# Kernel optimization log

Hardware: AMD Instinct MI355X
Metric: run time of the kernel (lower is better)

## Reference

```python
import jax, jax.numpy as jnp
import numpy as np

N, E = 20000, 320000
IN, HID, R, HEADS = 128, 256, 4, 4
C = HID // HEADS  # per-head dim


def setup_inputs() -> dict:
    key = jax.random.key(0)
    ks = jax.random.split(key, 20)
    g = lambda k, s, sc=0.05: jax.random.normal(k, s, jnp.float32) * sc
    return {
        'x': g(ks[0], (N, IN), 1.0),
        'edge_index': jax.random.randint(ks[1], (2, E), 0, N),
        'edge_type': jax.random.randint(ks[2], (E,), 0, R),
        'h_prev': g(ks[3], (N, HID), 1.0),
        # RGCN layer 1: relation weights, root weight, bias
        'W1': g(ks[4], (R, IN, HID)), 'root1': g(ks[5], (IN, HID)), 'b1': jnp.zeros((HID,), jnp.float32),
        # RGCN layer 2
        'W2': g(ks[6], (R, HID, HID)), 'root2': g(ks[7], (HID, HID)), 'b2': jnp.zeros((HID,), jnp.float32),
        # TransformerConv linears (query/key/value/skip), each Linear(HID, HEADS*C)
        'Wq': g(ks[8], (HID, HID)), 'bq': jnp.zeros((HID,), jnp.float32),
        'Wk': g(ks[9], (HID, HID)), 'bk': jnp.zeros((HID,), jnp.float32),
        'Wv': g(ks[10], (HID, HID)), 'bv': jnp.zeros((HID,), jnp.float32),
        'Wskip': g(ks[11], (HID, HID)), 'bskip': jnp.zeros((HID,), jnp.float32),
        # GRUCell (torch layout: [3*HID, in], gates ordered r, z, n)
        'W_ih': g(ks[12], (3 * HID, HID)), 'b_ih': jnp.zeros((3 * HID,), jnp.float32),
        'W_hh': g(ks[13], (3 * HID, HID)), 'b_hh': jnp.zeros((3 * HID,), jnp.float32),
    }


def rgcn(x, src, dst, etype, W, Wroot, b):
    # PyG RGCNConv: out_i = x_i @ Wroot + b + sum_r mean_{j in N_r(i)} x_j @ W_r
    n = x.shape[0]
    out = x @ Wroot + b
    xs = x[src]  # [E, F_in]
    for r in range(W.shape[0]):  # small fixed relation count
        mask = (etype == r).astype(x.dtype)  # [E]
        msg = (xs @ W[r]) * mask[:, None]  # [E, F_out]
        agg = jax.ops.segment_sum(msg, dst, num_segments=n)
        cnt = jax.ops.segment_sum(mask, dst, num_segments=n)
        out = out + agg / jnp.maximum(cnt, 1.0)[:, None]
    return out


def transformer_conv(x, src, dst, Wq, bq, Wk, bk, Wv, bv, Wskip, bskip):
    # PyG TransformerConv, concat=True, root_weight=True
    n = x.shape[0]
    q = (x @ Wq + bq).reshape(n, HEADS, C)
    k = (x @ Wk + bk).reshape(n, HEADS, C)
    v = (x @ Wv + bv).reshape(n, HEADS, C)
    score = jnp.einsum('ehc,ehc->eh', q[dst], k[src]) * (1.0 / np.sqrt(C))  # [E, H]
    smax = jax.ops.segment_max(score, dst, num_segments=n)  # [N, H]
    ex = jnp.exp(score - smax[dst])
    denom = jax.ops.segment_sum(ex, dst, num_segments=n)
    alpha = ex / jnp.maximum(denom[dst], 1e-16)  # edge softmax per dst node
    out = jax.ops.segment_sum(alpha[:, :, None] * v[src], dst, num_segments=n)  # [N, H, C]
    return out.reshape(n, HEADS * C) + x @ Wskip + bskip


def gru_cell(xi, h, W_ih, b_ih, W_hh, b_hh):
    gi = xi @ W_ih.T + b_ih
    gh = h @ W_hh.T + b_hh
    ir, iz, inn = jnp.split(gi, 3, axis=1)
    hr, hz, hn = jnp.split(gh, 3, axis=1)
    r = jax.nn.sigmoid(ir + hr)
    z = jax.nn.sigmoid(iz + hz)
    nw = jnp.tanh(inn + r * hn)
    return (1.0 - z) * nw + z * h


def reference(x, edge_index, edge_type, h_prev, W1, root1, b1, W2, root2, b2,
              Wq, bq, Wk, bk, Wv, bv, Wskip, bskip, W_ih, b_ih, W_hh, b_hh):
    src, dst = edge_index[0], edge_index[1]
    h = jax.nn.relu(rgcn(x, src, dst, edge_type, W1, root1, b1))
    h = jax.nn.relu(rgcn(h, src, dst, edge_type, W2, root2, b2))
    h = transformer_conv(h, src, dst, Wq, bq, Wk, bk, Wv, bv, Wskip, bskip)
    h = gru_cell(h, h_prev, W_ih, b_ih, W_hh, b_hh)
    return h
```

## Files before the change

### kernel.cpp

```cpp
#include <hip/hip_runtime.h>
#include <hip/hip_bf16.h>
#include <stdint.h>

#define N_NODES 20000
#define E_EDGES 320000
#define IN_F    128
#define HIDF    256
#define R_REL   4
#define NRKEYS  (N_NODES*R_REL)
#define SCAN_BLOCKS 80

typedef __attribute__((ext_vector_type(8))) short  short8;
typedef __attribute__((ext_vector_type(4))) float  floatx4;

__device__ __forceinline__ float bf2f(__hip_bfloat16 v){ return __bfloat162float(v); }
__device__ __forceinline__ __hip_bfloat16 f2bf(float v){ return __float2bfloat16(v); }
__device__ __forceinline__ float bfbits2f(unsigned short u){ return __uint_as_float(((unsigned)u)<<16); }
__device__ __forceinline__ unsigned short f2bfbits(float v){
    __hip_bfloat16 h = __float2bfloat16(v);
    return *(unsigned short*)&h;
}
__device__ __forceinline__ unsigned pack_bf2(float a, float b){
    return (unsigned)f2bfbits(a) | ((unsigned)f2bfbits(b) << 16);
}

__device__ __forceinline__ void gload_lds16(const void* g, void* l)
{
    __builtin_amdgcn_global_load_lds((const __attribute__((address_space(1))) void*)g,
                                     (__attribute__((address_space(3))) void*)l, 16, 0, 0);
}

__global__ void count_kernel(const int* __restrict__ ei, const int* __restrict__ et,
                             int* __restrict__ cnt)
{
    int e = blockIdx.x*256 + threadIdx.x;
    if (e >= E_EDGES) return;
    int dst = ei[E_EDGES + e];
    atomicAdd(&cnt[dst*R_REL + et[e]], 1);
}

__global__ __launch_bounds__(1024) void scan_reduce_kernel(const int* __restrict__ cnt,
                                                           int* __restrict__ blocksum)
{
    int ix = blockIdx.x*1024 + threadIdx.x;
    int v = (ix < NRKEYS) ? cnt[ix] : 0;
    #pragma unroll
    for (int o=32;o>0;o>>=1) v += __shfl_xor(v, o, 64);
    __shared__ int wsum[16];
    int wave = threadIdx.x >> 6, lane = threadIdx.x & 63;
    if (lane == 0) wsum[wave] = v;
    __syncthreads();
    if (threadIdx.x == 0) {
        int s = 0;
        #pragma unroll
        for (int w=0;w<16;w++) s += wsum[w];
        blocksum[blockIdx.x] = s;
    }
}

__global__ __launch_bounds__(128) void scan_sums_kernel(const int* __restrict__ blocksum,
                                                        int* __restrict__ blockoff)
{
    __shared__ int s[128];
    int t = threadIdx.x;
    int v = (t < SCAN_BLOCKS) ? blocksum[t] : 0;
    s[t] = v; __syncthreads();
    for (int off=1; off<128; off<<=1) {
        int u = (t>=off) ? s[t-off] : 0;
        __syncthreads();
        s[t] += u;
        __syncthreads();
    }
    if (t < SCAN_BLOCKS) blockoff[t] = s[t] - v;
}

__global__ __launch_bounds__(1024) void scan_apply_kernel(const int* __restrict__ cnt,
                                                          const int* __restrict__ blockoff,
                                                          int* __restrict__ row_ptr,
                                                          int* __restrict__ cursor)
{
    __shared__ int s[1024];
    int t = threadIdx.x;
    int ix = blockIdx.x*1024 + t;
    int v = (ix < NRKEYS) ? cnt[ix] : 0;
    s[t] = v; __syncthreads();
    for (int off=1; off<1024; off<<=1) {
        int u = (t>=off) ? s[t-off] : 0;
        __syncthreads();
        s[t] += u;
        __syncthreads();
    }
    if (ix < NRKEYS) {
        int excl = blockoff[blockIdx.x] + s[t] - v;
        row_ptr[ix] = excl;
        cursor[ix]  = excl;
        if (ix == NRKEYS-1) row_ptr[NRKEYS] = excl + v;
    }
}

__global__ void fill_kernel(const int* __restrict__ ei, const int* __restrict__ et,
                            int* __restrict__ cursor, int* __restrict__ csr_src)
{
    int e = blockIdx.x*256 + threadIdx.x;
    if (e >= E_EDGES) return;
    int src = ei[e];
    int dst = ei[E_EDGES + e];
    int key = dst*R_REL + et[e];
    int pos = atomicAdd(&cursor[key], 1);
    csr_src[pos] = src;
}

__global__ void make_b1t(const float* __restrict__ root1,
                         const float* __restrict__ W1,
                         __hip_bfloat16* __restrict__ B1t)
{
    int idx = blockIdx.x*256 + threadIdx.x;
    if (idx >= 256*640) return;
    int n = idx / 640, k = idx % 640;
    float v;
    if (k < 128) v = root1[k*256 + n];
    else         v = W1[(k-128)*256 + n];
    B1t[idx] = f2bf(v);
}

__global__ void make_b2t(const float* __restrict__ root2,
                         const float* __restrict__ W2,
                         __hip_bfloat16* __restrict__ B2t)
{
    int idx = blockIdx.x*256 + threadIdx.x;
    if (idx >= 256*1280) return;
    int n = idx / 1280, k = idx % 1280;
    float v;
    if (k < 256) v = root2[k*256 + n];
    else         v = W2[(k-256)*256 + n];
    B2t[idx] = f2bf(v);
}

__global__ void make_b3t(const float* __restrict__ Wq, const float* __restrict__ Wk,
                         const float* __restrict__ Wv, const float* __restrict__ Wsk,
                         const float* __restrict__ bq, const float* __restrict__ bk,
                         const float* __restrict__ bv, const float* __restrict__ bsk,
                         __hip_bfloat16* __restrict__ B3t, float* __restrict__ bias3)
{
    int idx = blockIdx.x*256 + threadIdx.x;
    if (idx >= 1024*256) return;
    int n = idx / 256, k = idx % 256;
    int g = n >> 8, nn = n & 255;
    const float* W = (g==0)?Wq:(g==1)?Wk:(g==2)?Wv:Wsk;
    B3t[idx] = f2bf(W[k*256 + nn]);
    if (k == 0) {
        const float* B = (g==0)?bq:(g==1)?bk:(g==2)?bv:bsk;
        bias3[n] = B[nn];
    }
}

__global__ void cvt_f32_bf16(const float* __restrict__ in, __hip_bfloat16* __restrict__ out, int n)
{
    int i = blockIdx.x*256 + threadIdx.x;
    if (i < n) out[i] = f2bf(in[i]);
}

__global__ __launch_bounds__(256) void agg1_kernel(const float* __restrict__ x,
                                                   const int* __restrict__ row_ptr,
                                                   const int* __restrict__ csr_src,
                                                   __hip_bfloat16* __restrict__ A1)
{
    int b = blockIdx.x*4 + (threadIdx.x >> 6);
    int lane = threadIdx.x & 63;
    int i = b >> 2, r = b & 3;
    int e0 = row_ptr[b], e1 = row_ptr[b+1];
    float sx0=0.f,sy0=0.f, sx1=0.f,sy1=0.f, sx2=0.f,sy2=0.f, sx3=0.f,sy3=0.f;
    int e = e0;
    for (; e+4 <= e1; e += 4) {
        int i0=csr_src[e], i1=csr_src[e+1], i2=csr_src[e+2], i3=csr_src[e+3];
        float2 v0 = *(const float2*)(x + (size_t)i0*IN_F + lane*2);
        float2 v1 = *(const float2*)(x + (size_t)i1*IN_F + lane*2);
        float2 v2 = *(const float2*)(x + (size_t)i2*IN_F + lane*2);
        float2 v3 = *(const float2*)(x + (size_t)i3*IN_F + lane*2);
        sx0+=v0.x; sy0+=v0.y; sx1+=v1.x; sy1+=v1.y;
        sx2+=v2.x; sy2+=v2.y; sx3+=v3.x; sy3+=v3.y;
    }
    for (; e < e1; e++) {
        int i0 = csr_src[e];
        float2 v = *(const float2*)(x + (size_t)i0*IN_F + lane*2);
        sx0+=v.x; sy0+=v.y;
    }
    float sx = (sx0+sx1)+(sx2+sx3);
    float sy = (sy0+sy1)+(sy2+sy3);
    float inv = (e1>e0) ? 1.f/(float)(e1-e0) : 0.f;
    *(unsigned*)(A1 + (size_t)i*640 + 128 + r*128 + lane*2) = pack_bf2(sx*inv, sy*inv);
    if (r == 0) {
        float2 v = *(const float2*)(x + (size_t)i*IN_F + lane*2);
        *(unsigned*)(A1 + (size_t)i*640 + lane*2) = pack_bf2(v.x, v.y);
    }
}

__global__ __launch_bounds__(256) void agg2_kernel(const int* __restrict__ row_ptr,
                                                   const int* __restrict__ csr_src,
                                                   __hip_bfloat16* __restrict__ A2)
{
    int b = blockIdx.x*4 + (threadIdx.x >> 6);
    int lane = threadIdx.x & 63;
    int i = b >> 2, r = b & 3;
    int e0 = row_ptr[b], e1 = row_ptr[b+1];
    float a0=0.f,a1=0.f,a2=0.f,a3=0.f;
    float b0=0.f,b1=0.f,b2=0.f,b3=0.f;
    float c0=0.f,c1=0.f,c2=0.f,c3=0.f;
    float d0=0.f,d1=0.f,d2=0.f,d3=0.f;
    int e = e0;
    for (; e+4 <= e1; e += 4) {
        int i0=csr_src[e], i1=csr_src[e+1], i2=csr_src[e+2], i3=csr_src[e+3];
        ushort4 u0 = *(const ushort4*)(A2 + (size_t)i0*1280 + lane*4);
        ushort4 u1 = *(const ushort4*)(A2 + (size_t)i1*1280 + lane*4);
        ushort4 u2 = *(const ushort4*)(A2 + (size_t)i2*1280 + lane*4);
        ushort4 u3 = *(const ushort4*)(A2 + (size_t)i3*1280 + lane*4);
        a0+=bfbits2f(u0.x); a1+=bfbits2f(u0.y); a2+=bfbits2f(u0.z); a3+=bfbits2f(u0.w);
        b0+=bfbits2f(u1.x); b1+=bfbits2f(u1.y); b2+=bfbits2f(u1.z); b3+=bfbits2f(u1.w);
        c0+=bfbits2f(u2.x); c1+=bfbits2f(u2.y); c2+=bfbits2f(u2.z); c3+=bfbits2f(u2.w);
        d0+=bfbits2f(u3.x); d1+=bfbits2f(u3.y); d2+=bfbits2f(u3.z); d3+=bfbits2f(u3.w);
    }
    for (; e < e1; e++) {
        int i0 = csr_src[e];
        ushort4 u = *(const ushort4*)(A2 + (size_t)i0*1280 + lane*4);
        a0+=bfbits2f(u.x); a1+=bfbits2f(u.y); a2+=bfbits2f(u.z); a3+=bfbits2f(u.w);
    }
    float s0=(a0+b0)+(c0+d0), s1=(a1+b1)+(c1+d1), s2=(a2+b2)+(c2+d2), s3=(a3+b3)+(c3+d3);
    float inv = (e1>e0) ? 1.f/(float)(e1-e0) : 0.f;
    uint2 w;
    w.x = pack_bf2(s0*inv, s1*inv);
    w.y = pack_bf2(s2*inv, s3*inv);
    *(uint2*)(A2 + (size_t)i*1280 + 256 + r*256 + lane*4) = w;
}

template<int MI>
__device__ __forceinline__ void gemm_bt_body(const __hip_bfloat16* __restrict__ A, int lda,
                                             const __hip_bfloat16* __restrict__ Bt,
                                             const float* __restrict__ bias,
                                             __hip_bfloat16* __restrict__ C, int ldc,
                                             int M, int K, int relu,
                                             int tile_m, int tile_n,
                                             __hip_bfloat16* lds_a, __hip_bfloat16* lds_b)
{
    constexpr int A_ELEMS = MI*1024;
    const int tid  = threadIdx.x;
    const int wave = tid >> 6;
    const int lane = tid & 63;
    const int wm = wave >> 1, wn = wave & 1;
    const int fm = lane & 15;
    const int q  = lane >> 4;
    const int sw = (q ^ ((fm >> 1) & 3)) * 8;

    floatx4 acc[MI][4];
    #pragma unroll
    for (int i=0;i<MI;i++)
        #pragma unroll
        for (int j=0;j<4;j++) acc[i][j] = (floatx4){0.f,0.f,0.f,0.f};

    const int srow   = lane >> 2;
    const int schunk = lane & 3;
    size_t a_goff[MI/2];  __hip_bfloat16* a_ldst[MI/2];
    #pragma unroll
    for (int s = 0; s < MI/2; ++s) {
        int r = (s*4 + wave)*16 + srow;
        int c = schunk ^ ((r >> 1) & 3);
        a_goff[s] = (size_t)min(tile_m + r, M-1)*lda + c*8;
        a_ldst[s] = lds_a + (s*4 + wave)*512;
    }
    size_t b_goff[2];  __hip_bfloat16* b_ldst[2];
    #pragma unroll
    for (int s = 0; s < 2; ++s) {
        int r = (s*4 + wave)*16 + srow;
        int c = schunk ^ ((r >> 1) & 3);
        b_goff[s] = (size_t)(tile_n + r)*K + c*8;
        b_ldst[s] = lds_b + (s*4 + wave)*512;
    }

    const int nt = K >> 5;

    #pragma unroll
    for (int s = 0; s < MI/2; ++s) gload_lds16(A + a_goff[s], a_ldst[s]);
    #pragma unroll
    for (int s = 0; s < 2; ++s)    gload_lds16(Bt + b_goff[s], b_ldst[s]);
    asm volatile("s_waitcnt vmcnt(0)" ::: "memory");
    __builtin_amdgcn_s_barrier();

    int cur = 0;
    for (int t = 0; t < nt; ++t) {
        if (t + 1 < nt) {
            const int nb = cur ^ 1;
            const int kn = (t + 1) << 5;
            #pragma unroll
            for (int s = 0; s < MI/2; ++s)
                gload_lds16(A + a_goff[s] + kn, a_ldst[s] + nb*A_ELEMS);
            #pragma unroll
            for (int s = 0; s < 2; ++s)
                gload_lds16(Bt + b_goff[s] + kn, b_ldst[s] + nb*4096);
        }

        const __hip_bfloat16* la = lds_a + cur*A_ELEMS;
        const __hip_bfloat16* lb = lds_b + cur*4096;
        short8 afr[MI], bfr[4];
        #pragma unroll
        for (int i=0;i<MI;i++)
            afr[i] = *(const short8*)(la + (wm*(MI*16) + i*16 + fm)*32 + sw);
        #pragma unroll
        for (int j=0;j<4;j++)
            bfr[j] = *(const short8*)(lb + (wn*64 + j*16 + fm)*32 + sw);

        #pragma unroll
        for (int i=0;i<MI;i++)
            #pragma unroll
            for (int j=0;j<4;j++)
                acc[i][j] = __builtin_amdgcn_mfma_f32_16x16x32_bf16(afr[i], bfr[j], acc[i][j], 0,0,0);

        if (t + 1 < nt) {
            asm volatile("s_waitcnt vmcnt(0)" ::: "memory");
            __builtin_amdgcn_s_barrier();
            cur ^= 1;
        }
    }

    const int crow_base = tile_m + wm*(MI*16);
    const int ccol_base = tile_n + wn*64;
    #pragma unroll
    for (int i=0;i<MI;i++) {
        #pragma unroll
        for (int j=0;j<4;j++) {
            int c  = ccol_base + j*16 + fm;
            float bb = bias[c];
            #pragma unroll
            for (int rg=0; rg<4; rg++) {
                int r = crow_base + i*16 + q*4 + rg;
                if (r < M) {
                    float v = acc[i][j][rg] + bb;
                    if (relu) v = fmaxf(v, 0.f);
                    C[(size_t)r*ldc + c] = f2bf(v);
                }
            }
        }
    }
}

template<int MI>
__global__ __launch_bounds__(256) void gemm_bt_t(const __hip_bfloat16* __restrict__ A, int lda,
                                                 const __hip_bfloat16* __restrict__ Bt,
                                                 const float* __restrict__ bias,
                                                 __hip_bfloat16* __restrict__ C, int ldc,
                                                 int M, int K, int relu)
{
    __shared__ __align__(16) __hip_bfloat16 lds_a[2*MI*1024];
    __shared__ __align__(16) __hip_bfloat16 lds_b[2*4096];
    gemm_bt_body<MI>(A, lda, Bt, bias, C, ldc, M, K, relu,
                     blockIdx.x*(MI*32), blockIdx.y*128, lds_a, lds_b);
}

__global__ __launch_bounds__(256) void gemm_bt_dual(const __hip_bfloat16* __restrict__ A0,
                                                    const __hip_bfloat16* __restrict__ A1,
                                                    const __hip_bfloat16* __restrict__ Bt0,
                                                    const __hip_bfloat16* __restrict__ Bt1,
                                                    const float* __restrict__ bias0,
                                                    const float* __restrict__ bias1,
                                                    __hip_bfloat16* __restrict__ C0,
                                                    __hip_bfloat16* __restrict__ C1)
{
    __shared__ __align__(16) __hip_bfloat16 lds_a[2*4096];
    __shared__ __align__(16) __hip_bfloat16 lds_b[2*4096];
    int which = blockIdx.y >= 6;
    int ty    = which ? (blockIdx.y - 6) : blockIdx.y;
    gemm_bt_body<4>(which ? A1 : A0, 256,
                    which ? Bt1 : Bt0,
                    which ? bias1 : bias0,
                    which ? C1 : C0, 768,
                    N_NODES, 256, 0,
                    blockIdx.x*128, ty*128, lds_a, lds_b);
}

__global__ __launch_bounds__(256) void score_kernel(const __hip_bfloat16* __restrict__ qkvs,
                                                    const int* __restrict__ row_ptr,
                                                    const int* __restrict__ csr_src,
                                                    float* __restrict__ score)
{
    int i = blockIdx.x*4 + (threadIdx.x >> 6);
    int lane = threadIdx.x & 63;
    int h = lane >> 4, d4 = lane & 15;
    int e0 = row_ptr[i*R_REL], e1 = row_ptr[i*R_REL + R_REL];
    ushort4 qv = *(const ushort4*)(qkvs + (size_t)i*1024 + lane*4);
    float qx=bfbits2f(qv.x), qy=bfbits2f(qv.y), qz=bfbits2f(qv.z), qw=bfbits2f(qv.w);
    float* sp = score + (size_t)h*E_EDGES;
    int j = e0;
    for (; j+2 <= e1; j += 2) {
        int s0 = csr_src[j], s1 = csr_src[j+1];
        ushort4 k0 = *(const ushort4*)(qkvs + (size_t)s0*1024 + 256 + lane*4);
        ushort4 k1 = *(const ushort4*)(qkvs + (size_t)s1*1024 + 256 + lane*4);
        float d0 = qx*bfbits2f(k0.x)+qy*bfbits2f(k0.y)+qz*bfbits2f(k0.z)+qw*bfbits2f(k0.w);
        float d1 = qx*bfbits2f(k1.x)+qy*bfbits2f(k1.y)+qz*bfbits2f(k1.z)+qw*bfbits2f(k1.w);
        #pragma unroll
        for (int o=1;o<16;o<<=1){ d0 += __shfl_xor(d0,o,64); d1 += __shfl_xor(d1,o,64); }
        if (d4 == 0) { sp[j] = d0*0.125f; sp[j+1] = d1*0.125f; }
    }
    for (; j < e1; j++) {
        int s0 = csr_src[j];
        ushort4 k0 = *(const ushort4*)(qkvs + (size_t)s0*1024 + 256 + lane*4);
        float d0 = qx*bfbits2f(k0.x)+qy*bfbits2f(k0.y)+qz*bfbits2f(k0.z)+qw*bfbits2f(k0.w);
        #pragma unroll
        for (int o=1;o<16;o<<=1) d0 += __shfl_xor(d0,o,64);
        if (d4 == 0) sp[j] = d0*0.125f;
    }
}

__global__ __launch_bounds__(256) void attn_agg_kernel(const __hip_bfloat16* __restrict__ qkvs,
                                                       const float* __restrict__ score,
                                                       const int* __restrict__ row_ptr,
                                                       const int* __restrict__ csr_src,
                                                       __hip_bfloat16* __restrict__ hatt)
{
    int i = blockIdx.x*4 + (threadIdx.x >> 6);
    int lane = threadIdx.x & 63;
    int h  = lane >> 4;
    int d4 = lane & 15;
    int e0 = row_ptr[i*R_REL], e1 = row_ptr[i*R_REL + R_REL];
    int deg = e1 - e0;
    const float* sp = score + (size_t)h*E_EDGES + e0;

    float m = -1e30f;
    for (int j = d4; j < deg; j += 16) m = fmaxf(m, sp[j]);
    #pragma unroll
    for (int o=1;o<16;o<<=1) m = fmaxf(m, __shfl_xor(m, o, 64));

    float ssum = 0.f;
    for (int j = d4; j < deg; j += 16) ssum += __expf(sp[j] - m);
    #pragma unroll
    for (int o=1;o<16;o<<=1) ssum += __shfl_xor(ssum, o, 64);
    float inv = 1.f / fmaxf(ssum, 1e-16f);

    float ax=0.f, ay=0.f, az=0.f, aw=0.f;
    int j = 0;
    for (; j+4 <= deg; j += 4) {
        int s0=csr_src[e0+j], s1=csr_src[e0+j+1], s2=csr_src[e0+j+2], s3=csr_src[e0+j+3];
        float w0 = __expf(sp[j]   - m) * inv;
        float w1 = __expf(sp[j+1] - m) * inv;
        float w2 = __expf(sp[j+2] - m) * inv;
        float w3 = __expf(sp[j+3] - m) * inv;
        ushort4 u0 = *(const ushort4*)(qkvs + (size_t)s0*1024 + 512 + lane*4);
        ushort4 u1 = *(const ushort4*)(qkvs + (size_t)s1*1024 + 512 + lane*4);
        ushort4 u2 = *(const ushort4*)(qkvs + (size_t)s2*1024 + 512 + lane*4);
        ushort4 u3 = *(const ushort4*)(qkvs + (size_t)s3*1024 + 512 + lane*4);
        ax += w0*bfbits2f(u0.x) + w1*bfbits2f(u1.x) + w2*bfbits2f(u2.x) + w3*bfbits2f(u3.x);
        ay += w0*bfbits2f(u0.y) + w1*bfbits2f(u1.y) + w2*bfbits2f(u2.y) + w3*bfbits2f(u3.y);
        az += w0*bfbits2f(u0.z) + w1*bfbits2f(u1.z) + w2*bfbits2f(u2.z) + w3*bfbits2f(u3.z);
        aw += w0*bfbits2f(u0.w) + w1*bfbits2f(u1.w) + w2*bfbits2f(u2.w) + w3*bfbits2f(u3.w);
    }
    for (; j < deg; j++) {
        int s = csr_src[e0+j];
        float w = __expf(sp[j] - m) * inv;
        ushort4 u = *(const ushort4*)(qkvs + (size_t)s*1024 + 512 + lane*4);
        ax += w*bfbits2f(u.x); ay += w*bfbits2f(u.y);
        az += w*bfbits2f(u.z); aw += w*bfbits2f(u.w);
    }
    ushort4 sk = *(const ushort4*)(qkvs + (size_t)i*1024 + 768 + lane*4);
    uint2 w;
    w.x = pack_bf2(ax + bfbits2f(sk.x), ay + bfbits2f(sk.y));
    w.y = pack_bf2(az + bfbits2f(sk.z), aw + bfbits2f(sk.w));
    *(uint2*)(hatt + (size_t)i*256 + lane*4) = w;
}

__global__ void gru_kernel(const __hip_bfloat16* __restrict__ gi,
                           const __hip_bfloat16* __restrict__ gh,
                           const float* __restrict__ hprev,
                           float* __restrict__ out)
{
    int idx = blockIdx.x*256 + threadIdx.x;
    if (idx >= N_NODES*HIDF) return;
    int i = idx / HIDF, c = idx % HIDF;
    size_t gb = (size_t)i*768;
    float ir = bf2f(gi[gb + c]), iz = bf2f(gi[gb + 256 + c]), in = bf2f(gi[gb + 512 + c]);
    float hr = bf2f(gh[gb + c]), hz = bf2f(gh[gb + 256 + c]), hn = bf2f(gh[gb + 512 + c]);
    float r = 1.f/(1.f + __expf(-(ir+hr)));
    float z = 1.f/(1.f + __expf(-(iz+hz)));
    float n = tanhf(in + r*hn);
    float h = hprev[idx];
    out[idx] = (1.f - z)*n + z*h;
}

extern "C" void kernel_launch(void* const* d_in, const int* in_sizes, int n_in,
                              void* d_out, int out_size, void* d_ws, size_t ws_size,
                              hipStream_t stream)
{
    const float* x       = (const float*)d_in[0];
    const int* edge_index= (const int*)d_in[1];
    const int* edge_type = (const int*)d_in[2];
    const float* hprev   = (const float*)d_in[3];
    const float* W1      = (const float*)d_in[4];
    const float* root1   = (const float*)d_in[5];
    const float* b1      = (const float*)d_in[6];
    const float* W2      = (const float*)d_in[7];
    const float* root2   = (const float*)d_in[8];
    const float* b2      = (const float*)d_in[9];
    const float* Wq      = (const float*)d_in[10];
    const float* bq      = (const float*)d_in[11];
    const float* Wk      = (const float*)d_in[12];
    const float* bk      = (const float*)d_in[13];
    const float* Wv      = (const float*)d_in[14];
    const float* bv      = (const float*)d_in[15];
    const float* Wskip   = (const float*)d_in[16];
    const float* bskip   = (const float*)d_in[17];
    const float* W_ih    = (const float*)d_in[18];
    const float* b_ih    = (const float*)d_in[19];
    const float* W_hh    = (const float*)d_in[20];
    const float* b_hh    = (const float*)d_in[21];

    char* ws = (char*)d_ws;
    size_t off = 0;
    auto take = [&](size_t bytes)->char* {
        char* p = ws + off;
        off = (off + bytes + 255) & ~(size_t)255;
        return p;
    };
    int* cnt        = (int*)take((size_t)NRKEYS*4);
    int* row_ptr    = (int*)take((size_t)(NRKEYS+1)*4);
    int* cursor     = (int*)take((size_t)NRKEYS*4);
    int* csr_src    = (int*)take((size_t)E_EDGES*4);
    int* blocksum   = (int*)take((size_t)SCAN_BLOCKS*4);
    int* blockoff   = (int*)take((size_t)(SCAN_BLOCKS+1)*4);
    float* score    = (float*)take((size_t)R_REL*E_EDGES*4);
    __hip_bfloat16* B1t   = (__hip_bfloat16*)take((size_t)256*640*2);
    __hip_bfloat16* B2t   = (__hip_bfloat16*)take((size_t)256*1280*2);
    __hip_bfloat16* B3t   = (__hip_bfloat16*)take((size_t)1024*256*2);
    __hip_bfloat16* Biht  = (__hip_bfloat16*)take((size_t)768*256*2);
    __hip_bfloat16* Bhht  = (__hip_bfloat16*)take((size_t)768*256*2);
    float*          bias3 = (float*)take((size_t)1024*4);
    __hip_bfloat16* hprev_bf = (__hip_bfloat16*)take((size_t)N_NODES*256*2);
    char* P1 = take((size_t)N_NODES*640*2);
    char* P2 = take((size_t)N_NODES*1536*2);

    __hip_bfloat16* A1   = (__hip_bfloat16*)P1;
    __hip_bfloat16* h2   = (__hip_bfloat16*)P1;
    __hip_bfloat16* hatt = (__hip_bfloat16*)P1;
    __hip_bfloat16* A2   = (__hip_bfloat16*)P2;
    __hip_bfloat16* qkvs = (__hip_bfloat16*)P2;
    __hip_bfloat16* gi   = (__hip_bfloat16*)P2;
    __hip_bfloat16* gh   = (__hip_bfloat16*)(P2 + (size_t)N_NODES*768*2);

    hipMemsetAsync(cnt, 0, (size_t)NRKEYS*4, stream);
    count_kernel<<<(E_EDGES+255)/256, 256, 0, stream>>>(edge_index, edge_type, cnt);
    scan_reduce_kernel<<<SCAN_BLOCKS, 1024, 0, stream>>>(cnt, blocksum);
    scan_sums_kernel<<<1, 128, 0, stream>>>(blocksum, blockoff);
    scan_apply_kernel<<<SCAN_BLOCKS, 1024, 0, stream>>>(cnt, blockoff, row_ptr, cursor);
    fill_kernel<<<(E_EDGES+255)/256, 256, 0, stream>>>(edge_index, edge_type, cursor, csr_src);

    make_b1t<<<(256*640+255)/256, 256, 0, stream>>>(root1, W1, B1t);
    make_b2t<<<(256*1280+255)/256, 256, 0, stream>>>(root2, W2, B2t);
    make_b3t<<<(1024*256+255)/256, 256, 0, stream>>>(Wq, Wk, Wv, Wskip, bq, bk, bv, bskip, B3t, bias3);
    cvt_f32_bf16<<<(768*256+255)/256, 256, 0, stream>>>(W_ih, Biht, 768*256);
    cvt_f32_bf16<<<(768*256+255)/256, 256, 0, stream>>>(W_hh, Bhht, 768*256);
    cvt_f32_bf16<<<(N_NODES*256+255)/256, 256, 0, stream>>>(hprev, hprev_bf, N_NODES*256);

    agg1_kernel<<<NRKEYS/4, 256, 0, stream>>>(x, row_ptr, csr_src, A1);

    dim3 g12(313, 2);
    gemm_bt_t<2><<<g12, 256, 0, stream>>>(A1, 640, B1t, b1, A2, 1280, N_NODES, 640, 1);

    agg2_kernel<<<NRKEYS/4, 256, 0, stream>>>(row_ptr, csr_src, A2);

    gemm_bt_t<2><<<g12, 256, 0, stream>>>(A2, 1280, B2t, b2, h2, 256, N_NODES, 1280, 1);

    dim3 g3(157, 8);
    gemm_bt_t<4><<<g3, 256, 0, stream>>>(h2, 256, B3t, bias3, qkvs, 1024, N_NODES, 256, 0);

    score_kernel<<<N_NODES/4, 256, 0, stream>>>(qkvs, row_ptr, csr_src, score);
    attn_agg_kernel<<<N_NODES/4, 256, 0, stream>>>(qkvs, score, row_ptr, csr_src, hatt);

    dim3 g45(157, 12);
    gemm_bt_dual<<<g45, 256, 0, stream>>>(hatt, hprev_bf, Biht, Bhht, b_ih, b_hh, gi, gh);

    gru_kernel<<<(N_NODES*HIDF+255)/256, 256, 0, stream>>>(gi, gh, hprev, (float*)d_out);
}
```

Measured before the change: 450.5 us.

## Triple-buffer GEMM LDS pipeline, add XCD block swizzle and MFMA priority

Moves the bf16 GEMM mainloop from double to triple buffering. Tile t+2 is issued while tile t computes, and the wait becomes a partial vmcnt so only the oldest tile's loads are awaited. Blocks are remapped across the 8 XCDs so neighbouring tiles share an L2, and s_setprio is raised around the MFMA burst. The cost is more LDS per block, which may reduce occupancy, and the remap adds a little index arithmetic.

```diff
diff --git a/kernel.cpp b/kernel.cpp
--- a/kernel.cpp
+++ b/kernel.cpp
@@ -28,6 +28,26 @@
 {
     __builtin_amdgcn_global_load_lds((const __attribute__((address_space(1))) void*)g,
                                      (__attribute__((address_space(3))) void*)l, 16, 0, 0);
+}
+
+template<int N>
+__device__ __forceinline__ void wait_vm()
+{
+    if constexpr (N == 0)      asm volatile("s_waitcnt vmcnt(0)" ::: "memory");
+    else if constexpr (N == 3) asm volatile("s_waitcnt vmcnt(3)" ::: "memory");
+    else if constexpr (N == 4) asm volatile("s_waitcnt vmcnt(4)" ::: "memory");
+    else                       asm volatile("s_waitcnt vmcnt(0)" ::: "memory");
+}
+
+__device__ __forceinline__ int2 xcd_swizzle()
+{
+    int gx = gridDim.x, gy = gridDim.y;
+    int nwg = gx * gy;
+    int lin = blockIdx.x + gx * blockIdx.y;
+    int q = nwg >> 3, r = nwg & 7;
+    int k = lin & 7, i = lin >> 3;
+    int j = (k < r ? k*(q+1) : r*(q+1) + (k-r)*q) + i;
+    return make_int2(j / gy, j % gy);
 }
 
 __global__ void count_kernel(const int* __restrict__ ei, const int* __restrict__ et,
@@ -242,6 +262,8 @@
                                              __hip_bfloat16* lds_a, __hip_bfloat16* lds_b)
 {
     constexpr int A_ELEMS = MI*1024;
+    constexpr int B_ELEMS = 4096;
+    constexpr int L = MI/2 + 2;
     const int tid  = threadIdx.x;
     const int wave = tid >> 6;
     const int lane = tid & 63;
@@ -258,47 +280,44 @@
 
     const int srow   = lane >> 2;
     const int schunk = lane & 3;
-    size_t a_goff[MI/2];  __hip_bfloat16* a_ldst[MI/2];
+    size_t a_goff[MI/2];
     #pragma unroll
     for (int s = 0; s < MI/2; ++s) {
         int r = (s*4 + wave)*16 + srow;
         int c = schunk ^ ((r >> 1) & 3);
         a_goff[s] = (size_t)min(tile_m + r, M-1)*lda + c*8;
-        a_ldst[s] = lds_a + (s*4 + wave)*512;
-    }
-    size_t b_goff[2];  __hip_bfloat16* b_ldst[2];
+    }
+    size_t b_goff[2];
     #pragma unroll
     for (int s = 0; s < 2; ++s) {
         int r = (s*4 + wave)*16 + srow;
         int c = schunk ^ ((r >> 1) & 3);
         b_goff[s] = (size_t)(tile_n + r)*K + c*8;
-        b_ldst[s] = lds_b + (s*4 + wave)*512;
     }
 
     const int nt = K >> 5;
 
-    #pragma unroll
-    for (int s = 0; s < MI/2; ++s) gload_lds16(A + a_goff[s], a_ldst[s]);
-    #pragma unroll
-    for (int s = 0; s < 2; ++s)    gload_lds16(Bt + b_goff[s], b_ldst[s]);
-    asm volatile("s_waitcnt vmcnt(0)" ::: "memory");
+    auto issue = [&](int t, int bufi) {
+        const int kn = t << 5;
+        #pragma unroll
+        for (int s = 0; s < MI/2; ++s)
+            gload_lds16(A + a_goff[s] + kn, lds_a + bufi*A_ELEMS + (s*4 + wave)*512);
+        #pragma unroll
+        for (int s = 0; s < 2; ++s)
+            gload_lds16(Bt + b_goff[s] + kn, lds_b + bufi*B_ELEMS + (s*4 + wave)*512);
+    };
+
+    issue(0, 0);
+    if (nt > 1) { issue(1, 1); wait_vm<L>(); }
+    else        { wait_vm<0>(); }
     __builtin_amdgcn_s_barrier();
 
-    int cur = 0;
+    int cur = 0, nx2 = 2;
     for (int t = 0; t < nt; ++t) {
-        if (t + 1 < nt) {
-            const int nb = cur ^ 1;
-            const int kn = (t + 1) << 5;
-            #pragma unroll
-            for (int s = 0; s < MI/2; ++s)
-                gload_lds16(A + a_goff[s] + kn, a_ldst[s] + nb*A_ELEMS);
-            #pragma unroll
-            for (int s = 0; s < 2; ++s)
-                gload_lds16(Bt + b_goff[s] + kn, b_ldst[s] + nb*4096);
-        }
+        if (t + 2 < nt) issue(t + 2, nx2);
 
         const __hip_bfloat16* la = lds_a + cur*A_ELEMS;
-        const __hip_bfloat16* lb = lds_b + cur*4096;
+        const __hip_bfloat16* lb = lds_b + cur*B_ELEMS;
         short8 afr[MI], bfr[4];
         #pragma unroll
         for (int i=0;i<MI;i++)
@@ -307,16 +326,20 @@
         for (int j=0;j<4;j++)
             bfr[j] = *(const short8*)(lb + (wn*64 + j*16 + fm)*32 + sw);
 
+        __builtin_amdgcn_s_setprio(1);
         #pragma unroll
         for (int i=0;i<MI;i++)
             #pragma unroll
             for (int j=0;j<4;j++)
                 acc[i][j] = __builtin_amdgcn_mfma_f32_16x16x32_bf16(afr[i], bfr[j], acc[i][j], 0,0,0);
+        __builtin_amdgcn_s_setprio(0);
 
         if (t + 1 < nt) {
-            asm volatile("s_waitcnt vmcnt(0)" ::: "memory");
+            if (t + 2 < nt) wait_vm<L>();
+            else            wait_vm<0>();
             __builtin_amdgcn_s_barrier();
-            cur ^= 1;
+            cur = (cur == 2) ? 0 : cur + 1;
+            nx2 = (nx2 == 2) ? 0 : nx2 + 1;
         }
     }
 
@@ -348,10 +371,11 @@
                                                  __hip_bfloat16* __restrict__ C, int ldc,
                                                  int M, int K, int relu)
 {
-    __shared__ __align__(16) __hip_bfloat16 lds_a[2*MI*1024];
-    __shared__ __align__(16) __hip_bfloat16 lds_b[2*4096];
+    __shared__ __align__(16) __hip_bfloat16 lds_a[3*MI*1024];
+    __shared__ __align__(16) __hip_bfloat16 lds_b[3*4096];
+    int2 xy = xcd_swizzle();
     gemm_bt_body<MI>(A, lda, Bt, bias, C, ldc, M, K, relu,
-                     blockIdx.x*(MI*32), blockIdx.y*128, lds_a, lds_b);
+                     xy.x*(MI*32), xy.y*128, lds_a, lds_b);
 }
 
 __global__ __launch_bounds__(256) void gemm_bt_dual(const __hip_bfloat16* __restrict__ A0,
@@ -363,16 +387,17 @@
                                                     __hip_bfloat16* __restrict__ C0,
                                                     __hip_bfloat16* __restrict__ C1)
 {
-    __shared__ __align__(16) __hip_bfloat16 lds_a[2*4096];
-    __shared__ __align__(16) __hip_bfloat16 lds_b[2*4096];
-    int which = blockIdx.y >= 6;
-    int ty    = which ? (blockIdx.y - 6) : blockIdx.y;
+    __shared__ __align__(16) __hip_bfloat16 lds_a[3*4096];
+    __shared__ __align__(16) __hip_bfloat16 lds_b[3*4096];
+    int2 xy = xcd_swizzle();
+    int which = xy.y >= 6;
+    int ty    = which ? (xy.y - 6) : xy.y;
     gemm_bt_body<4>(which ? A1 : A0, 256,
                     which ? Bt1 : Bt0,
                     which ? bias1 : bias0,
                     which ? C1 : C0, 768,
                     N_NODES, 256, 0,
-                    blockIdx.x*128, ty*128, lds_a, lds_b);
+                    xy.x*128, ty*128, lds_a, lds_b);
 }
 
 __global__ __launch_bounds__(256) void score_kernel(const __hip_bfloat16* __restrict__ qkvs,
```

New measurement: 434.1 us. 1.04x faster.
